# Kernel optimization log

Measured on AMD Instinct MI355X. Metric: run time of the kernel, lower is better.

The kernel has to match this reference:

```python
import jax, jax.numpy as jnp
import numpy as np


def setup_inputs() -> dict:
    key = jax.random.key(0)
    ks = jax.random.split(key, 6)
    B, C, S = 256, 2048, 7          # batch, embed_dim, spacial_dim
    OUT = 1024                      # output_dim
    return {
        "x": jax.random.normal(ks[0], (B, C, S, S), jnp.float32),
        "pos_emb": jax.random.normal(ks[1], (S * S + 1, C), jnp.float32) / (C ** 0.5),
        "Wv": jax.random.normal(ks[2], (C, C), jnp.float32) * 0.02,
        "bv": jnp.zeros((C,), jnp.float32),
        "Wc": jax.random.normal(ks[3], (OUT, C), jnp.float32) * 0.02,
        "bc": jnp.zeros((OUT,), jnp.float32),
        "num_heads": 32,
    }


def reference(x, pos_emb, Wv, bv, Wc, bc, num_heads):
    # x: [B, C, H, W] -> tokens [B, HW, C], prepend mean token -> [B, N, C]
    B, C, H, W = x.shape
    N = H * W + 1
    hd = C // num_heads
    scale = hd ** -0.5

    t = x.reshape(B, C, H * W).transpose(0, 2, 1)                    # [B, HW, C]
    t = jnp.concatenate([t.mean(axis=1, keepdims=True), t], axis=1)  # [B, N, C]
    t = t + pos_emb[None]                                            # add pos emb

    # qkv weights are all copies of v_proj => q = k = v = v_proj(t)
    v = t @ Wv.T + bv                                                # [B, N, C]
    vh = v.reshape(B, N, num_heads, hd).transpose(0, 2, 1, 3)        # [B, h, N, d]

    # attn_ori = softmax(q k^T * scale) with q=k=v; dropout p=0 (eval)
    attn = jax.nn.softmax(jnp.einsum('bhnd,bhmd->bhnm', vh, vh) * scale, axis=-1)
    ctx = jnp.einsum('bhnm,bhmd->bhnd', attn, vh)                    # [B, h, N, d]
    ctx = ctx.transpose(0, 2, 1, 3).reshape(B, N, C)

    # proj weights come from c_proj: [out_dim, C]
    x_ori = ctx @ Wc.T + bc                                          # [B, N, out]
    xout = v @ Wc.T + bc                                             # x-path: proj(v) directly
    # x[:, 0, :] = x_ori[:, 0, :]; module returns x (first list element)
    return xout.at[:, 0, :].set(x_ori[:, 0, :])
```

## Files before the change

### kernel.cpp

```cpp
#include <hip/hip_runtime.h>
#include <stdint.h>

#define BATCH  256
#define CDIM   2048
#define HW     49
#define NTOK   50
#define MROWS  (BATCH * NTOK)
#define ODIM   1024
#define NHEADS 32

typedef __attribute__((ext_vector_type(8))) short short8;
typedef __attribute__((ext_vector_type(4))) float f32x4;
typedef unsigned short u16;
typedef unsigned int   u32;

__device__ __forceinline__ float bf2f(u16 u) {
  union { u32 i; float f; } v; v.i = ((u32)u) << 16; return v.f;
}
__device__ __forceinline__ u16 f2bf(float f) {
  union { float f; u32 i; } v; v.f = f;
  u32 r = v.i + 0x7fffu + ((v.i >> 16) & 1u);
  return (u16)(r >> 16);
}

__device__ __forceinline__ void async16(const void* g, void* l) {
  __builtin_amdgcn_global_load_lds(
      (const __attribute__((address_space(1))) u32*)g,
      (__attribute__((address_space(3))) u32*)l, 16, 0, 0);
}

#define BARRIER() asm volatile("s_barrier" ::: "memory")

__global__ __launch_bounds__(256) void cvt_prep_kernel(
    const float* __restrict__ Wv, u16* __restrict__ WvB, int n4a,
    const float* __restrict__ Wc, u16* __restrict__ WcB, int n4b,
    const float* __restrict__ x, const float* __restrict__ pos,
    u16* __restrict__ T, int nCvt) {
  if (blockIdx.x < (unsigned)nCvt) {
    int i = blockIdx.x * 256 + threadIdx.x;
    const float* src; u16* dst; int idx;
    if (i < n4a) { src = Wv; dst = WvB; idx = i; }
    else {
      idx = i - n4a;
      if (idx >= n4b) return;
      src = Wc; dst = WcB;
    }
    float4 v = reinterpret_cast<const float4*>(src)[idx];
    ushort4 o;
    o.x = f2bf(v.x); o.y = f2bf(v.y); o.z = f2bf(v.z); o.w = f2bf(v.w);
    reinterpret_cast<ushort4*>(dst)[idx] = o;
    return;
  }
  const int blk = blockIdx.x - nCvt;
  const int b  = blk >> 5;
  const int c0 = (blk & 31) * 64;
  __shared__ float xs[64 * HW];
  __shared__ float mean[64];
  const float* src = x + ((size_t)b * CDIM + c0) * HW;
  for (int i = threadIdx.x; i < 64 * HW / 4; i += 256)
    reinterpret_cast<float4*>(xs)[i] = reinterpret_cast<const float4*>(src)[i];
  __syncthreads();
  if (threadIdx.x < 64) {
    float s = 0.f;
#pragma unroll
    for (int j = 0; j < HW; j++) s += xs[threadIdx.x * HW + j];
    mean[threadIdx.x] = s * (1.0f / 49.0f);
  }
  __syncthreads();
  for (int wi = threadIdx.x; wi < NTOK * 8; wi += 256) {
    const int n = wi >> 3;
    const int g = (wi & 7) * 8;
    alignas(16) u16 ov[8];
#pragma unroll
    for (int u = 0; u < 8; u++) {
      const int c = g + u;
      float val = (n == 0) ? mean[c] : xs[c * HW + (n - 1)];
      val += pos[n * CDIM + c0 + c];
      ov[u] = f2bf(val);
    }
    *reinterpret_cast<uint4*>(&T[((size_t)b * NTOK + n) * CDIM + c0 + g]) =
        *reinterpret_cast<const uint4*>(ov);
  }
}

template<int OUT_BF16>
__global__ __launch_bounds__(512, 2)
void gemm256(const u16* __restrict__ A, const u16* __restrict__ Bm,
             const float* __restrict__ bias, void* __restrict__ Cout,
             int M, int N, int K, int nbx) {
  __shared__ __align__(16) u16 smem[65536];

  const int NK = K >> 6;
  const int t = threadIdx.x;
  const int lane = t & 63;
  const int wid = t >> 6;
  const int wm = wid >> 2;
  const int wn = wid & 3;

  const int nwg = gridDim.x;
  const int cpx = nwg >> 3;
  const int orig = blockIdx.x;
  const int swz = (orig & 7) * cpx + (orig >> 3);
  const int bx = swz % nbx;
  const int by = swz / nbx;
  const int m0 = by * 256, n0 = bx * 256;

  const int tr  = t >> 3;
  const int to8 = ((t & 7) ^ (tr & 7)) << 3;
  const int t8  = t << 3;
  const u16* pA0 = A  + (size_t)(m0 + tr) * K + to8;
  const u16* pB0 = Bm + (size_t)(n0 + tr) * K + to8;

  const int lr = lane & 15, hi = lane >> 4;
  const int sx = lr & 7;
  const int aK0 = ((wm * 128 + lr) << 6) + (((0 + hi) ^ sx) << 3);
  const int aK1 = ((wm * 128 + lr) << 6) + (((4 + hi) ^ sx) << 3);
  const int bK0 = 16384 + ((wn * 64 + lr) << 6) + (((0 + hi) ^ sx) << 3);
  const int bK1 = 16384 + ((wn * 64 + lr) << 6) + (((4 + hi) ^ sx) << 3);

  f32x4 acc[8][4] = {};
  short8 a[4][2], b[4][2];

  auto STG = [&](int kti, int isB, int h) {
    if (kti < NK) {
      const u16* g = (isB ? pB0 : pA0) + (size_t)(h * 128) * K + kti * 64;
      u16* l = &smem[((kti & 1) << 15) + (isB << 14) + (h << 13) + t8];
      async16(g, l);
      async16(g + (size_t)64 * K, l + 4096);
    }
  };

#define MFMA4x2(BN0, ACCM, ACCN)                                              \
  _Pragma("unroll")                                                           \
  for (int fm = 0; fm < 4; ++fm) {                                            \
    _Pragma("unroll")                                                         \
    for (int fn = 0; fn < 2; ++fn) {                                          \
      acc[(ACCM) + fm][(ACCN) + fn] = __builtin_amdgcn_mfma_f32_16x16x32_bf16(\
          a[fm][0], b[(BN0) + fn][0], acc[(ACCM) + fm][(ACCN) + fn], 0, 0, 0);\
      acc[(ACCM) + fm][(ACCN) + fn] = __builtin_amdgcn_mfma_f32_16x16x32_bf16(\
          a[fm][1], b[(BN0) + fn][1], acc[(ACCM) + fm][(ACCN) + fn], 0, 0, 0);\
    }                                                                         \
  }

  STG(0, 0, 0); STG(0, 0, 1); STG(0, 1, 0); STG(0, 1, 1);
  asm volatile("s_waitcnt vmcnt(0)" ::: "memory");
  BARRIER();

  for (int j = 0; j < NK; ++j) {
    const u16* sa = &smem[(j & 1) << 15];

#pragma unroll
    for (int f = 0; f < 4; ++f) {
      a[f][0] = *(const short8*)&sa[aK0 + f * 1024];
      a[f][1] = *(const short8*)&sa[aK1 + f * 1024];
    }
#pragma unroll
    for (int f = 0; f < 4; ++f) {
      b[f][0] = *(const short8*)&sa[bK0 + f * 1024];
      b[f][1] = *(const short8*)&sa[bK1 + f * 1024];
    }
    STG(j + 1, 0, 0); STG(j + 1, 0, 1); STG(j + 1, 1, 0); STG(j + 1, 1, 1);
    BARRIER();
    asm volatile("s_waitcnt lgkmcnt(0)" ::: "memory");
    __builtin_amdgcn_sched_barrier(0);
    __builtin_amdgcn_s_setprio(1);
    MFMA4x2(0, 0, 0);
    MFMA4x2(2, 0, 2);
    __builtin_amdgcn_s_setprio(0);
    BARRIER();

#pragma unroll
    for (int f = 0; f < 4; ++f) {
      a[f][0] = *(const short8*)&sa[aK0 + (4 + f) * 1024];
      a[f][1] = *(const short8*)&sa[aK1 + (4 + f) * 1024];
    }
    BARRIER();
    asm volatile("s_waitcnt lgkmcnt(0)" ::: "memory");
    __builtin_amdgcn_sched_barrier(0);
    __builtin_amdgcn_s_setprio(1);
    MFMA4x2(2, 4, 2);
    MFMA4x2(0, 4, 0);
    __builtin_amdgcn_s_setprio(0);
    asm volatile("s_waitcnt vmcnt(0)" ::: "memory");
    BARRIER();
  }

  const int erow = hi * 4;
#pragma unroll
  for (int fm = 0; fm < 8; ++fm) {
#pragma unroll
    for (int fn = 0; fn < 4; ++fn) {
      const int cg = n0 + wn * 64 + fn * 16 + lr;
      const float bb = bias[cg];
      const int rbase = m0 + wm * 128 + fm * 16 + erow;
#pragma unroll
      for (int jr = 0; jr < 4; ++jr) {
        const float val = acc[fm][fn][jr] + bb;
        if (OUT_BF16)
          ((u16*)Cout)[(size_t)(rbase + jr) * N + cg] = f2bf(val);
        else
          ((float*)Cout)[(size_t)(rbase + jr) * N + cg] = val;
      }
    }
  }
#undef MFMA4x2
}

__global__ __launch_bounds__(64) void attn0_kernel(u16* __restrict__ V) {
  const int b = blockIdx.x, h = blockIdx.y;
  __shared__ __align__(16) u16 vt[NTOK * 64];
  __shared__ float pb[64];
  const int t = threadIdx.x;
  u16* base = V + (size_t)b * NTOK * CDIM + h * 64;
  for (int idx = t; idx < NTOK * 8; idx += 64) {
    const int m = idx >> 3, g = (idx & 7) * 8;
    *reinterpret_cast<uint4*>(&vt[m * 64 + g]) =
        *reinterpret_cast<const uint4*>(base + (size_t)m * CDIM + g);
  }
  __syncthreads();
  const float qd = bf2f(vt[t]);
  float s_own = -1e30f;
  for (int m = 0; m < NTOK; m++) {
    float p = qd * bf2f(vt[m * 64 + t]);
#pragma unroll
    for (int off = 32; off; off >>= 1) p += __shfl_xor(p, off);
    if (t == m) s_own = p * 0.125f;
  }
  float mx = s_own;
#pragma unroll
  for (int off = 32; off; off >>= 1) mx = fmaxf(mx, __shfl_xor(mx, off));
  const float e = (t < NTOK) ? __expf(s_own - mx) : 0.f;
  float Z = e;
#pragma unroll
  for (int off = 32; off; off >>= 1) Z += __shfl_xor(Z, off);
  pb[t] = e / Z;
  __syncthreads();
  float acc = 0.f;
  for (int m = 0; m < NTOK; m++) acc += pb[m] * bf2f(vt[m * 64 + t]);
  base[t] = f2bf(acc);
}

extern "C" void kernel_launch(void* const* d_in, const int* in_sizes, int n_in,
                              void* d_out, int out_size, void* d_ws, size_t ws_size,
                              hipStream_t stream) {
  const float* x   = (const float*)d_in[0];
  const float* pos = (const float*)d_in[1];
  const float* Wv  = (const float*)d_in[2];
  const float* bv  = (const float*)d_in[3];
  const float* Wc  = (const float*)d_in[4];
  const float* bc  = (const float*)d_in[5];
  float* out = (float*)d_out;

  u16* T   = (u16*)d_ws;
  u16* V   = T   + (size_t)MROWS * CDIM;
  u16* WvB = V   + (size_t)MROWS * CDIM;
  u16* WcB = WvB + (size_t)CDIM * CDIM;

  {
    int n4a = CDIM * CDIM / 4;
    int n4b = ODIM * CDIM / 4;
    int nCvt = (n4a + n4b + 255) / 256;
    cvt_prep_kernel<<<nCvt + BATCH * 32, 256, 0, stream>>>(
        Wv, WvB, n4a, Wc, WcB, n4b, x, pos, T, nCvt);
  }

  gemm256<1><<<(MROWS / 256) * (CDIM / 256), 512, 0, stream>>>(
      T, WvB, bv, V, MROWS, CDIM, CDIM, CDIM / 256);

  attn0_kernel<<<dim3(BATCH, NHEADS), 64, 0, stream>>>(V);

  gemm256<0><<<(MROWS / 256) * (ODIM / 256), 512, 0, stream>>>(
      V, WcB, bc, out, MROWS, ODIM, CDIM, ODIM / 256);
}
```

Baseline: 288.0 us.

## Replace 256x256 double-buffered GEMM with simpler single-buffered 128x128 tile GEMM

```diff
diff --git a/kernel.cpp b/kernel.cpp
--- a/kernel.cpp
+++ b/kernel.cpp
@@ -84,18 +84,18 @@
 }
 
 template<int OUT_BF16>
-__global__ __launch_bounds__(512, 2)
-void gemm256(const u16* __restrict__ A, const u16* __restrict__ Bm,
+__global__ __launch_bounds__(256, 3)
+void gemm128(const u16* __restrict__ A, const u16* __restrict__ Bm,
              const float* __restrict__ bias, void* __restrict__ Cout,
              int M, int N, int K, int nbx) {
-  __shared__ __align__(16) u16 smem[65536];
+  __shared__ __align__(16) u16 smem[16384];
 
   const int NK = K >> 6;
   const int t = threadIdx.x;
   const int lane = t & 63;
   const int wid = t >> 6;
-  const int wm = wid >> 2;
-  const int wn = wid & 3;
+  const int wm = wid >> 1;
+  const int wn = wid & 1;
 
   const int nwg = gridDim.x;
   const int cpx = nwg >> 3;
@@ -103,7 +103,7 @@
   const int swz = (orig & 7) * cpx + (orig >> 3);
   const int bx = swz % nbx;
   const int by = swz / nbx;
-  const int m0 = by * 256, n0 = bx * 256;
+  const int m0 = by * 128, n0 = bx * 128;
 
   const int tr  = t >> 3;
   const int to8 = ((t & 7) ^ (tr & 7)) << 3;
@@ -113,86 +113,58 @@
 
   const int lr = lane & 15, hi = lane >> 4;
   const int sx = lr & 7;
-  const int aK0 = ((wm * 128 + lr) << 6) + (((0 + hi) ^ sx) << 3);
-  const int aK1 = ((wm * 128 + lr) << 6) + (((4 + hi) ^ sx) << 3);
-  const int bK0 = 16384 + ((wn * 64 + lr) << 6) + (((0 + hi) ^ sx) << 3);
-  const int bK1 = 16384 + ((wn * 64 + lr) << 6) + (((4 + hi) ^ sx) << 3);
-
-  f32x4 acc[8][4] = {};
+  const int aK0 = ((wm * 64 + lr) << 6) + (((0 + hi) ^ sx) << 3);
+  const int aK1 = ((wm * 64 + lr) << 6) + (((4 + hi) ^ sx) << 3);
+  const int bK0 = 8192 + ((wn * 64 + lr) << 6) + (((0 + hi) ^ sx) << 3);
+  const int bK1 = 8192 + ((wn * 64 + lr) << 6) + (((4 + hi) ^ sx) << 3);
+
+  f32x4 acc[4][4] = {};
   short8 a[4][2], b[4][2];
 
-  auto STG = [&](int kti, int isB, int h) {
-    if (kti < NK) {
-      const u16* g = (isB ? pB0 : pA0) + (size_t)(h * 128) * K + kti * 64;
-      u16* l = &smem[((kti & 1) << 15) + (isB << 14) + (h << 13) + t8];
-      async16(g, l);
-      async16(g + (size_t)64 * K, l + 4096);
-    }
-  };
-
-#define MFMA4x2(BN0, ACCM, ACCN)                                              \
-  _Pragma("unroll")                                                           \
-  for (int fm = 0; fm < 4; ++fm) {                                            \
-    _Pragma("unroll")                                                         \
-    for (int fn = 0; fn < 2; ++fn) {                                          \
-      acc[(ACCM) + fm][(ACCN) + fn] = __builtin_amdgcn_mfma_f32_16x16x32_bf16(\
-          a[fm][0], b[(BN0) + fn][0], acc[(ACCM) + fm][(ACCN) + fn], 0, 0, 0);\
-      acc[(ACCM) + fm][(ACCN) + fn] = __builtin_amdgcn_mfma_f32_16x16x32_bf16(\
-          a[fm][1], b[(BN0) + fn][1], acc[(ACCM) + fm][(ACCN) + fn], 0, 0, 0);\
-    }                                                                         \
-  }
-
-  STG(0, 0, 0); STG(0, 0, 1); STG(0, 1, 0); STG(0, 1, 1);
-  asm volatile("s_waitcnt vmcnt(0)" ::: "memory");
-  BARRIER();
-
-  for (int j = 0; j < NK; ++j) {
-    const u16* sa = &smem[(j & 1) << 15];
+  for (int kt = 0; kt < NK; ++kt) {
+#pragma unroll
+    for (int c = 0; c < 4; ++c)
+      async16(pA0 + (size_t)(c * 32) * K + kt * 64, &smem[c * 2048 + t8]);
+#pragma unroll
+    for (int c = 0; c < 4; ++c)
+      async16(pB0 + (size_t)(c * 32) * K + kt * 64, &smem[8192 + c * 2048 + t8]);
+    asm volatile("s_waitcnt vmcnt(0)" ::: "memory");
+    BARRIER();
 
 #pragma unroll
     for (int f = 0; f < 4; ++f) {
-      a[f][0] = *(const short8*)&sa[aK0 + f * 1024];
-      a[f][1] = *(const short8*)&sa[aK1 + f * 1024];
+      a[f][0] = *(const short8*)&smem[aK0 + f * 1024];
+      a[f][1] = *(const short8*)&smem[aK1 + f * 1024];
     }
 #pragma unroll
     for (int f = 0; f < 4; ++f) {
-      b[f][0] = *(const short8*)&sa[bK0 + f * 1024];
-      b[f][1] = *(const short8*)&sa[bK1 + f * 1024];
-    }
-    STG(j + 1, 0, 0); STG(j + 1, 0, 1); STG(j + 1, 1, 0); STG(j + 1, 1, 1);
-    BARRIER();
+      b[f][0] = *(const short8*)&smem[bK0 + f * 1024];
+      b[f][1] = *(const short8*)&smem[bK1 + f * 1024];
+    }
     asm volatile("s_waitcnt lgkmcnt(0)" ::: "memory");
     __builtin_amdgcn_sched_barrier(0);
     __builtin_amdgcn_s_setprio(1);
-    MFMA4x2(0, 0, 0);
-    MFMA4x2(2, 0, 2);
+#pragma unroll
+    for (int fm = 0; fm < 4; ++fm)
+#pragma unroll
+      for (int fn = 0; fn < 4; ++fn) {
+        acc[fm][fn] = __builtin_amdgcn_mfma_f32_16x16x32_bf16(
+            a[fm][0], b[fn][0], acc[fm][fn], 0, 0, 0);
+        acc[fm][fn] = __builtin_amdgcn_mfma_f32_16x16x32_bf16(
+            a[fm][1], b[fn][1], acc[fm][fn], 0, 0, 0);
+      }
     __builtin_amdgcn_s_setprio(0);
     BARRIER();
-
-#pragma unroll
-    for (int f = 0; f < 4; ++f) {
-      a[f][0] = *(const short8*)&sa[aK0 + (4 + f) * 1024];
-      a[f][1] = *(const short8*)&sa[aK1 + (4 + f) * 1024];
-    }
-    BARRIER();
-    asm volatile("s_waitcnt lgkmcnt(0)" ::: "memory");
-    __builtin_amdgcn_sched_barrier(0);
-    __builtin_amdgcn_s_setprio(1);
-    MFMA4x2(2, 4, 2);
-    MFMA4x2(0, 4, 0);
-    __builtin_amdgcn_s_setprio(0);
-    asm volatile("s_waitcnt vmcnt(0)" ::: "memory");
-    BARRIER();
   }
 
   const int erow = hi * 4;
 #pragma unroll
-  for (int fm = 0; fm < 8; ++fm) {
+  for (int fm = 0; fm < 4; ++fm) {
 #pragma unroll
     for (int fn = 0; fn < 4; ++fn) {
       const int cg = n0 + wn * 64 + fn * 16 + lr;
       const float bb = bias[cg];
-      const int rbase = m0 + wm * 128 + fm * 16 + erow;
+      const int rbase = m0 + wm * 64 + fm * 16 + erow;
 #pragma unroll
       for (int jr = 0; jr < 4; ++jr) {
         const float val = acc[fm][fn][jr] + bb;
@@ -203,7 +175,6 @@
       }
     }
   }
-#undef MFMA4x2
 }
 
 __global__ __launch_bounds__(64) void attn0_kernel(u16* __restrict__ V) {
@@ -264,11 +235,11 @@
         Wv, WvB, n4a, Wc, WcB, n4b, x, pos, T, nCvt);
   }
 
-  gemm256<1><<<(MROWS / 256) * (CDIM / 256), 512, 0, stream>>>(
-      T, WvB, bv, V, MROWS, CDIM, CDIM, CDIM / 256);
+  gemm128<1><<<(MROWS / 128) * (CDIM / 128), 256, 0, stream>>>(
+      T, WvB, bv, V, MROWS, CDIM, CDIM, CDIM / 128);
 
   attn0_kernel<<<dim3(BATCH, NHEADS), 64, 0, stream>>>(V);
 
-  gemm256<0><<<(MROWS / 256) * (ODIM / 256), 512, 0, stream>>>(
-      V, WcB, bc, out, MROWS, ODIM, CDIM, ODIM / 256);
-}
+  gemm128<0><<<(MROWS / 128) * (ODIM / 128), 256, 0, stream>>>(
+      V, WcB, bc, out, MROWS, ODIM, CDIM, ODIM / 128);
+}
```

Measured after the change: 311.8 us. +8.3%, slower.
